# Kernel tuning notes

Hardware: AMD Instinct MI355X
Metric: run time of the kernel (lower is better)

The kernel has to match this reference:

```python
import jax, jax.numpy as jnp
import numpy as np

B, N, S, D1, D2 = 8, 8192, 2048, 128, 256
MLP = [256, 128]
IN_CH = D1 + D2
EPS_INTERP = 1e-8
EPS_BN = 1e-5


def setup_inputs() -> dict:
    key = jax.random.key(0)
    ks = jax.random.split(key, 12)
    inp = {
        "xyz1": jax.random.normal(ks[0], (B, 3, N), dtype=jnp.float32),
        "xyz2": jax.random.normal(ks[1], (B, 3, S), dtype=jnp.float32),
        "points1": jax.random.normal(ks[2], (B, D1, N), dtype=jnp.float32),
        "points2": jax.random.normal(ks[3], (B, D2, S), dtype=jnp.float32),
    }
    # Conv1d(k=1) weights are [out, in]; BN has gamma/beta per channel.
    last = IN_CH
    for i, oc in enumerate(MLP):
        inp[f"W{i}"] = jax.random.normal(ks[4 + 2 * i], (oc, last), dtype=jnp.float32) * (1.0 / np.sqrt(last))
        inp[f"b{i}"] = jnp.zeros((oc,), dtype=jnp.float32)
        inp[f"g{i}"] = jnp.ones((oc,), dtype=jnp.float32)
        inp[f"be{i}"] = jnp.zeros((oc,), dtype=jnp.float32)
        last = oc
    return inp


def _interpolate(xyz1, xyz2, points2):
    # xyz1: [B,3,N] -> [B,N,3]; xyz2: [B,3,S] -> [B,S,3]; points2: [B,D2,S] -> [B,S,D2]
    x1 = jnp.transpose(xyz1, (0, 2, 1))
    x2 = jnp.transpose(xyz2, (0, 2, 1))
    p2 = jnp.transpose(points2, (0, 2, 1))
    # squared distances [B,N,S]
    dists = (jnp.sum(x1 * x1, -1)[:, :, None]
             - 2.0 * jnp.einsum("bnc,bsc->bns", x1, x2)
             + jnp.sum(x2 * x2, -1)[:, None, :])
    neg_d, idx = jax.lax.top_k(-dists, 3)         # 3 nearest neighbors
    d = -neg_d                                     # [B,N,3]
    recip = 1.0 / (d + EPS_INTERP)
    weight = recip / jnp.sum(recip, axis=2, keepdims=True)
    gathered = jax.vmap(lambda p, i: p[i])(p2, idx)   # [B,N,3,D2]
    return jnp.sum(gathered * weight[..., None], axis=2)  # [B,N,D2]


def _conv_bn_relu(x, W, b, g, be):
    # x: [B,C,N]; 1x1 conv == channel GEMM
    y = jnp.einsum("oc,bcn->bon", W, x) + b[None, :, None]
    mean = jnp.mean(y, axis=(0, 2), keepdims=True)
    var = jnp.mean((y - mean) ** 2, axis=(0, 2), keepdims=True)  # biased, torch BN train
    y = (y - mean) * jax.lax.rsqrt(var + EPS_BN)
    y = y * g[None, :, None] + be[None, :, None]
    return jax.nn.relu(y)


def reference(xyz1, xyz2, points1, points2, W0, b0, g0, be0, W1, b1, g1, be1):
    interp = _interpolate(xyz1, xyz2, points2)               # [B,N,D2]
    p1 = jnp.transpose(points1, (0, 2, 1))                    # [B,N,D1]
    new_points = jnp.concatenate([p1, interp], axis=-1)       # [B,N,D1+D2]
    new_points = jnp.transpose(new_points, (0, 2, 1))         # [B,D1+D2,N]
    new_points = _conv_bn_relu(new_points, W0, b0, g0, be0)
    new_points = _conv_bn_relu(new_points, W1, b1, g1, be1)
    return new_points
```

## Files before the change

### kernel.cpp

```cpp
#include <hip/hip_runtime.h>

typedef unsigned short ushort_t;
typedef __bf16 bf16x8 __attribute__((ext_vector_type(8)));
typedef float floatx4 __attribute__((ext_vector_type(4)));
typedef unsigned short ushort8_t __attribute__((ext_vector_type(8)));

#define B_ 8
#define N_ 8192
#define S_ 2048
#define D1_ 128
#define D2_ 256
#define INCH_ 384
#define M_ 65536

#define ASYNC_CP16(g, l)                                                  \
  __builtin_amdgcn_global_load_lds(                                       \
      (const __attribute__((address_space(1))) void*)(g),                 \
      (__attribute__((address_space(3))) void*)(l), 16, 0, 0)

constexpr size_t OFF_STATS = 0;
constexpr size_t OFF_W0B   = 8192;
constexpr size_t OFF_W1B   = 204800;
constexpr size_t OFF_X2P   = 270336;
constexpr size_t OFF_P2T   = 532480;
constexpr size_t OFF_XC    = 8921088;
constexpr size_t OFF_Y1    = 59252736;
constexpr size_t OFF_PS0   = OFF_P2T;
constexpr size_t OFF_PQ0   = OFF_P2T + 1048576;
constexpr size_t OFF_PS1   = OFF_P2T + 2097152;
constexpr size_t OFF_PQ1   = OFF_P2T + 2621440;

__device__ __forceinline__ ushort_t f2bf(float f) {
  __bf16 h = (__bf16)f;
  union { __bf16 h; ushort_t u; } v;
  v.h = h;
  return v.u;
}
__device__ __forceinline__ float bf2f(ushort_t h) {
  return __uint_as_float(((unsigned int)h) << 16);
}

__device__ __forceinline__ void ins3(float e, int s,
                                     float& c0, float& c1, float& c2,
                                     int& i0, int& i1, int& i2) {
  bool l0 = e < c0, l1 = e < c1, l2 = e < c2;
  float nf0 = fminf(e, c0);
  float nf1 = __builtin_amdgcn_fmed3f(e, c0, c1);
  float nf2 = __builtin_amdgcn_fmed3f(e, c1, c2);
  i2 = l1 ? i1 : (l2 ? s : i2);
  i1 = l0 ? i0 : (l1 ? s : i1);
  i0 = l0 ? s : i0;
  c0 = nf0; c1 = nf1; c2 = nf2;
}

__global__ __launch_bounds__(256) void k_pre(const float* __restrict__ W0,
                                             const float* __restrict__ W1,
                                             const float* __restrict__ xyz2,
                                             const float* __restrict__ P2,
                                             const float* __restrict__ P1,
                                             ushort_t* __restrict__ W0b,
                                             ushort_t* __restrict__ W1b,
                                             float4* __restrict__ x2p,
                                             ushort_t* __restrict__ p2t,
                                             ushort_t* __restrict__ Xc) {
  __shared__ float t[32][33];
  const int blk = blockIdx.x;
  const int tid = threadIdx.x;
  if (blk < 576) {
    int i = blk * 256 + tid;
    if (i < 98304) {
      W0b[i] = f2bf(W0[i]);
    } else if (i < 131072) {
      W1b[i - 98304] = f2bf(W1[i - 98304]);
    } else {
      int idx = i - 131072;
      int b = idx >> 11, s = idx & (S_ - 1);
      const float* base = xyz2 + (size_t)b * 3 * S_;
      float x = base[s], y = base[S_ + s], z = base[2 * S_ + s];
      x2p[idx] = make_float4(x, y, z, 0.5f * (x * x + y * y + z * z));
    }
    return;
  }
  int tx = tid & 31, ty = tid >> 5;
  if (blk < 4672) {
    int idx = blk - 576;
    int s0 = (idx & 63) * 32;
    int c0 = ((idx >> 6) & 7) * 32;
    int b = idx >> 9;
#pragma unroll
    for (int j = 0; j < 4; j++) {
      int c = c0 + ty + j * 8;
      t[ty + j * 8][tx] = P2[((size_t)b * D2_ + c) * S_ + s0 + tx];
    }
    __syncthreads();
#pragma unroll
    for (int j = 0; j < 4; j++) {
      int s = s0 + ty + j * 8;
      p2t[((size_t)b * S_ + s) * D2_ + c0 + tx] = f2bf(t[tx][ty + j * 8]);
    }
  } else {
    int idx = blk - 4672;
    int n0 = (idx & 255) * 32;
    int c0 = ((idx >> 8) & 3) * 32;
    int b = idx >> 10;
#pragma unroll
    for (int j = 0; j < 4; j++) {
      int c = c0 + ty + j * 8;
      t[ty + j * 8][tx] = P1[((size_t)b * D1_ + c) * N_ + n0 + tx];
    }
    __syncthreads();
#pragma unroll
    for (int j = 0; j < 4; j++) {
      int n = n0 + ty + j * 8;
      Xc[((size_t)b * N_ + n) * INCH_ + c0 + tx] = f2bf(t[tx][ty + j * 8]);
    }
  }
}

__global__ __launch_bounds__(512, 8) void k_knn(const float* __restrict__ xyz1,
                                                const float4* __restrict__ x2p,
                                                const ushort_t* __restrict__ p2t,
                                                ushort_t* __restrict__ Xc) {
  __shared__ float4 xs[8 * 289];
  __shared__ float wsh[64 * 3];
  __shared__ int   ish[64 * 3];
  int t = threadIdx.x;
  int q0 = blockIdx.x * 64;
  int b = q0 >> 13;
  int n0 = q0 & (N_ - 1);
  for (int l = t; l < S_; l += 512)
    xs[(l >> 8) * 289 + (l & 255)] = x2p[(size_t)b * S_ + l];
  int sub = t & 7;
  int qg = t >> 3;
  int n = n0 + qg;
  float qx = xyz1[((size_t)b * 3 + 0) * N_ + n];
  float qy = xyz1[((size_t)b * 3 + 1) * N_ + n];
  float qz = xyz1[((size_t)b * 3 + 2) * N_ + n];
  float nrm1 = qx * qx + qy * qy + qz * qz;
  __syncthreads();
  const float4* bp = xs + sub * 289;
  float k0 = 3e38f, k1 = 3e38f, k2 = 3e38f, k3 = 3e38f;
#pragma unroll 4
  for (int i = 0; i < 256; ++i) {
    float4 P = bp[i];
    float e = fmaf(-qx, P.x, fmaf(-qy, P.y, fmaf(-qz, P.z, P.w)));
    float dd = fmaf(2.f, e, nrm1);
    unsigned int kb = (__float_as_uint(dd) & 0xFFFFFF00u) | (unsigned int)i;
    float k = __uint_as_float(kb);
    float n0_ = fminf(k, k0);
    float n1_ = __builtin_amdgcn_fmed3f(k, k0, k1);
    float n2_ = __builtin_amdgcn_fmed3f(k, k1, k2);
    float n3_ = __builtin_amdgcn_fmed3f(k, k2, k3);
    k0 = n0_; k1 = n1_; k2 = n2_; k3 = n3_;
  }
  float ed[4];
  int   si[4];
  {
    float kk[4] = {k0, k1, k2, k3};
#pragma unroll
    for (int c = 0; c < 4; ++c) {
      int loc = (int)(__float_as_uint(kk[c]) & 255u);
      float4 P = bp[loc];
      float e = fmaf(-qx, P.x, fmaf(-qy, P.y, fmaf(-qz, P.z, P.w)));
      ed[c] = fmaf(2.f, e, nrm1);
      si[c] = (sub << 8) + loc;
    }
  }
  float c0 = 3e38f, c1 = 3e38f, c2 = 3e38f;
  int i0 = 0, i1 = 0, i2 = 0;
#pragma unroll
  for (int c = 0; c < 4; ++c) ins3(ed[c], si[c], c0, c1, c2, i0, i1, i2);
#pragma unroll
  for (int d = 1; d < 8; d <<= 1) {
    float e0 = __shfl_xor(c0, d); int s0 = __shfl_xor(i0, d);
    float e1 = __shfl_xor(c1, d); int s1 = __shfl_xor(i1, d);
    float e2 = __shfl_xor(c2, d); int s2 = __shfl_xor(i2, d);
    ins3(e0, s0, c0, c1, c2, i0, i1, i2);
    ins3(e1, s1, c0, c1, c2, i0, i1, i2);
    ins3(e2, s2, c0, c1, c2, i0, i1, i2);
  }
  if (sub == 0) {
    float r0 = 1.f / (c0 + 1e-8f);
    float r1 = 1.f / (c1 + 1e-8f);
    float r2 = 1.f / (c2 + 1e-8f);
    float rs = 1.f / (r0 + r1 + r2);
    wsh[qg * 3 + 0] = r0 * rs; wsh[qg * 3 + 1] = r1 * rs; wsh[qg * 3 + 2] = r2 * rs;
    ish[qg * 3 + 0] = i0; ish[qg * 3 + 1] = i1; ish[qg * 3 + 2] = i2;
  }
  __syncthreads();
  int lane = t & 63, grp = t >> 6;
  size_t sbase2 = (size_t)b * S_;
#pragma unroll 2
  for (int it = 0; it < 8; ++it) {
    int ql = it * 8 + grp;
    int q = q0 + ql;
    float w0 = wsh[ql * 3 + 0], w1 = wsh[ql * 3 + 1], w2 = wsh[ql * 3 + 2];
    int j0 = ish[ql * 3 + 0], j1 = ish[ql * 3 + 1], j2 = ish[ql * 3 + 2];
    ushort4 a0 = *(const ushort4*)&p2t[(sbase2 + j0) * D2_ + lane * 4];
    ushort4 a1 = *(const ushort4*)&p2t[(sbase2 + j1) * D2_ + lane * 4];
    ushort4 a2 = *(const ushort4*)&p2t[(sbase2 + j2) * D2_ + lane * 4];
    ushort4 o;
    o.x = f2bf(w0 * bf2f(a0.x) + w1 * bf2f(a1.x) + w2 * bf2f(a2.x));
    o.y = f2bf(w0 * bf2f(a0.y) + w1 * bf2f(a1.y) + w2 * bf2f(a2.y));
    o.z = f2bf(w0 * bf2f(a0.z) + w1 * bf2f(a1.z) + w2 * bf2f(a2.z));
    o.w = f2bf(w0 * bf2f(a0.w) + w1 * bf2f(a1.w) + w2 * bf2f(a2.w));
    *(ushort4*)&Xc[(size_t)q * INCH_ + D1_ + lane * 4] = o;
  }
}

__global__ __launch_bounds__(256) void k_redstats(const float* __restrict__ ps,
                                                  const float* __restrict__ pq,
                                                  float* __restrict__ sum,
                                                  float* __restrict__ ssq,
                                                  int ncols, int nrows) {
  __shared__ float ls[4], lq[4];
  int col = blockIdx.x;
  int t = threadIdx.x;
  float s = 0.f, q = 0.f;
  for (int r = t; r < nrows; r += 256) {
    s += ps[(size_t)r * ncols + col];
    q += pq[(size_t)r * ncols + col];
  }
#pragma unroll
  for (int d = 1; d < 64; d <<= 1) {
    s += __shfl_xor(s, d);
    q += __shfl_xor(q, d);
  }
  if ((t & 63) == 0) { ls[t >> 6] = s; lq[t >> 6] = q; }
  __syncthreads();
  if (t == 0) {
    sum[col] = ls[0] + ls[1] + ls[2] + ls[3];
    ssq[col] = lq[0] + lq[1] + lq[2] + lq[3];
  }
}

__global__ __launch_bounds__(256, 4) void k_gemm1(const ushort_t* __restrict__ A,
                                                  const ushort_t* __restrict__ Bw,
                                                  ushort_t* __restrict__ Cc,
                                                  float* __restrict__ psum,
                                                  float* __restrict__ pssq) {
  __shared__ __align__(16) char g1buf[20480];
  __shared__ float red_s[2][256], red_q[2][256];
  ushort_t* As = (ushort_t*)g1buf;
  ushort_t* Bs = (ushort_t*)(g1buf + 4096);
  ushort_t* cs = (ushort_t*)g1buf;
  const int tid = threadIdx.x;
  const int m0 = blockIdx.x * 64;
  const int wave = tid >> 6;
  const int wuni = __builtin_amdgcn_readfirstlane(wave);
  const int lane = tid & 63;
  const int quad = lane >> 4;
  const int l16 = lane & 15;
  const int wrow = (wave >> 1) * 32;
  const int wcol = (wave & 1) * 128;
  const int arow = tid >> 2, aseg = tid & 3;
  floatx4 acc[2][8];
#pragma unroll
  for (int i = 0; i < 2; i++)
#pragma unroll
    for (int j = 0; j < 8; j++) acc[i][j] = (floatx4){0.f, 0.f, 0.f, 0.f};

  for (int k0 = 0; k0 < INCH_; k0 += 32) {
    ASYNC_CP16(&A[(size_t)(m0 + arow) * INCH_ + k0 + aseg * 8], &As[wuni * 512]);
#pragma unroll
    for (int it = 0; it < 4; it++) {
      int l = tid + it * 256;
      int row = l >> 2, seg = l & 3;
      ASYNC_CP16(&Bw[(size_t)row * INCH_ + k0 + seg * 8], &Bs[it * 2048 + wuni * 512]);
    }
    __syncthreads();
    bf16x8 af[2];
#pragma unroll
    for (int mt = 0; mt < 2; mt++) af[mt] = *(const bf16x8*)&As[(wrow + mt * 16 + l16) * 32 + quad * 8];
#pragma unroll
    for (int half = 0; half < 2; half++) {
      bf16x8 bfr[4];
#pragma unroll
      for (int j = 0; j < 4; j++) {
        int nt = half * 4 + j;
        bfr[j] = *(const bf16x8*)&Bs[(wcol + nt * 16 + l16) * 32 + quad * 8];
      }
#pragma unroll
      for (int mt = 0; mt < 2; mt++)
#pragma unroll
        for (int j = 0; j < 4; j++)
          acc[mt][half * 4 + j] =
              __builtin_amdgcn_mfma_f32_16x16x32_bf16(af[mt], bfr[j], acc[mt][half * 4 + j], 0, 0, 0);
    }
    __syncthreads();
  }
#pragma unroll
  for (int nt = 0; nt < 8; nt++) {
    float s = 0.f, s2 = 0.f;
#pragma unroll
    for (int mt = 0; mt < 2; mt++)
#pragma unroll
      for (int i = 0; i < 4; i++) {
        float v = acc[mt][nt][i];
        s += v;
        s2 = fmaf(v, v, s2);
      }
    s += __shfl_xor(s, 16);  s2 += __shfl_xor(s2, 16);
    s += __shfl_xor(s, 32);  s2 += __shfl_xor(s2, 32);
    if (quad == 0) {
      int col = wcol + nt * 16 + l16;
      red_s[wave >> 1][col] = s;
      red_q[wave >> 1][col] = s2;
    }
  }
#pragma unroll
  for (int h = 0; h < 2; ++h) {
    __syncthreads();
    if ((wave & 1) == h) {
#pragma unroll
      for (int mt = 0; mt < 2; mt++)
#pragma unroll
        for (int i = 0; i < 4; i++) {
          int rl = wrow + mt * 16 + quad * 4 + i;
#pragma unroll
          for (int nt = 0; nt < 8; nt++)
            cs[rl * 136 + nt * 16 + l16] = f2bf(acc[mt][nt][i]);
        }
    }
    __syncthreads();
#pragma unroll
    for (int v = 0; v < 4; ++v) {
      int idx = v * 256 + tid;
      int row = idx >> 4;
      int c8 = (idx & 15) * 8;
      ushort8_t val = *(const ushort8_t*)&cs[row * 136 + c8];
      *(ushort8_t*)&Cc[(size_t)(m0 + row) * 256 + h * 128 + c8] = val;
    }
  }
  __syncthreads();
  {
    psum[(size_t)blockIdx.x * 256 + tid] = red_s[0][tid] + red_s[1][tid];
    pssq[(size_t)blockIdx.x * 256 + tid] = red_q[0][tid] + red_q[1][tid];
  }
}

__global__ __launch_bounds__(256, 4) void k_gemm2t(const ushort_t* __restrict__ Y1,
                                                   const ushort_t* __restrict__ Bw,
                                                   const float* __restrict__ sum0,
                                                   const float* __restrict__ ssq0,
                                                   const float* __restrict__ g0,
                                                   const float* __restrict__ be0,
                                                   ushort_t* __restrict__ Y2t,
                                                   float* __restrict__ psum,
                                                   float* __restrict__ pssq) {
  __shared__ __align__(16) char ubuf[64 * 129 * 4];
  __shared__ float scs[256], shs[256];
  __shared__ float red_s[2][128], red_q[2][128];
  ushort_t* As = (ushort_t*)ubuf;
  ushort_t* Bs = (ushort_t*)(ubuf + 4096);
  float* tb = (float*)ubuf;
  const int tid = threadIdx.x;
  const int m0 = blockIdx.x * 64;
  const int b = m0 >> 13;
  const int n0 = m0 & (N_ - 1);
  const int wave = tid >> 6;
  const int wuni = __builtin_amdgcn_readfirstlane(wave);
  const int lane = tid & 63;
  const int quad = lane >> 4;
  const int l16 = lane & 15;
  const int wrow = (wave >> 1) * 32;
  const int wcol = (wave & 1) * 64;
  {
    float mean = sum0[tid] * (1.f / 65536.f);
    float var = ssq0[tid] * (1.f / 65536.f) - mean * mean;
    float sc = rsqrtf(var + 1e-5f) * g0[tid];
    scs[tid] = sc;
    shs[tid] = be0[tid] - mean * sc;
  }
  floatx4 acc[2][4];
#pragma unroll
  for (int i = 0; i < 2; i++)
#pragma unroll
    for (int j = 0; j < 4; j++) acc[i][j] = (floatx4){0.f, 0.f, 0.f, 0.f};
  __syncthreads();

  const int arow = tid >> 2, aseg = tid & 3;
  for (int k0 = 0; k0 < 256; k0 += 32) {
#pragma unroll
    for (int it = 0; it < 2; it++) {
      int l = tid + it * 256;
      int row = l >> 2, seg = l & 3;
      ASYNC_CP16(&Bw[(size_t)row * 256 + k0 + seg * 8], &Bs[it * 2048 + wuni * 512]);
    }
    {
      ushort4 y01 = *(const ushort4*)&Y1[(size_t)(m0 + arow) * 256 + k0 + aseg * 8];
      ushort4 y23 = *(const ushort4*)&Y1[(size_t)(m0 + arow) * 256 + k0 + aseg * 8 + 4];
      int c = k0 + aseg * 8;
      ushort4 o0, o1;
      o0.x = f2bf(fmaxf(fmaf(bf2f(y01.x), scs[c + 0], shs[c + 0]), 0.f));
      o0.y = f2bf(fmaxf(fmaf(bf2f(y01.y), scs[c + 1], shs[c + 1]), 0.f));
      o0.z = f2bf(fmaxf(fmaf(bf2f(y01.z), scs[c + 2], shs[c + 2]), 0.f));
      o0.w = f2bf(fmaxf(fmaf(bf2f(y01.w), scs[c + 3], shs[c + 3]), 0.f));
      o1.x = f2bf(fmaxf(fmaf(bf2f(y23.x), scs[c + 4], shs[c + 4]), 0.f));
      o1.y = f2bf(fmaxf(fmaf(bf2f(y23.y), scs[c + 5], shs[c + 5]), 0.f));
      o1.z = f2bf(fmaxf(fmaf(bf2f(y23.z), scs[c + 6], shs[c + 6]), 0.f));
      o1.w = f2bf(fmaxf(fmaf(bf2f(y23.w), scs[c + 7], shs[c + 7]), 0.f));
      *(ushort4*)&As[arow * 32 + aseg * 8] = o0;
      *(ushort4*)&As[arow * 32 + aseg * 8 + 4] = o1;
    }
    __syncthreads();
    bf16x8 af[2], bfr[4];
#pragma unroll
    for (int mt = 0; mt < 2; mt++) af[mt] = *(const bf16x8*)&As[(wrow + mt * 16 + l16) * 32 + quad * 8];
#pragma unroll
    for (int nt = 0; nt < 4; nt++) bfr[nt] = *(const bf16x8*)&Bs[(wcol + nt * 16 + l16) * 32 + quad * 8];
#pragma unroll
    for (int mt = 0; mt < 2; mt++)
#pragma unroll
      for (int nt = 0; nt < 4; nt++)
        acc[mt][nt] = __builtin_amdgcn_mfma_f32_16x16x32_bf16(af[mt], bfr[nt], acc[mt][nt], 0, 0, 0);
    __syncthreads();
  }
#pragma unroll
  for (int nt = 0; nt < 4; nt++) {
    float s = 0.f, s2 = 0.f;
#pragma unroll
    for (int mt = 0; mt < 2; mt++)
#pragma unroll
      for (int i = 0; i < 4; i++) {
        float v = acc[mt][nt][i];
        s += v;
        s2 = fmaf(v, v, s2);
      }
    s += __shfl_xor(s, 16);  s2 += __shfl_xor(s2, 16);
    s += __shfl_xor(s, 32);  s2 += __shfl_xor(s2, 32);
    if (quad == 0) {
      int col = wcol + nt * 16 + l16;
      red_s[wave >> 1][col] = s;
      red_q[wave >> 1][col] = s2;
    }
  }
#pragma unroll
  for (int mt = 0; mt < 2; mt++)
#pragma unroll
    for (int i = 0; i < 4; i++) {
      int rl = wrow + mt * 16 + quad * 4 + i;
#pragma unroll
      for (int nt = 0; nt < 4; nt++) {
        int col = wcol + nt * 16 + l16;
        tb[rl * 129 + col] = acc[mt][nt][i];
      }
    }
  __syncthreads();
  if (tid < 128) {
    psum[(size_t)blockIdx.x * 128 + tid] = red_s[0][tid] + red_s[1][tid];
    pssq[(size_t)blockIdx.x * 128 + tid] = red_q[0][tid] + red_q[1][tid];
  }
#pragma unroll
  for (int v = 0; v < 4; ++v) {
    int idx = v * 256 + tid;
    int c = idx >> 3;
    int j8 = (idx & 7) * 8;
    ushort8_t val;
#pragma unroll
    for (int k = 0; k < 8; ++k) val[k] = f2bf(tb[(j8 + k) * 129 + c]);
    *(ushort8_t*)&Y2t[((size_t)(b * 128 + c)) * N_ + n0 + j8] = val;
  }
}

__global__ __launch_bounds__(256) void k_out2(const ushort_t* __restrict__ Y2t,
                                              const float* __restrict__ sum1,
                                              const float* __restrict__ ssq1,
                                              const float* __restrict__ g1,
                                              const float* __restrict__ be1,
                                              float* __restrict__ out) {
  __shared__ float sc1[128], sh1[128];
  int tid = threadIdx.x;
  if (tid < 128) {
    float mean = sum1[tid] * (1.f / 65536.f);
    float var = ssq1[tid] * (1.f / 65536.f) - mean * mean;
    float sc = rsqrtf(var + 1e-5f) * g1[tid];
    sc1[tid] = sc;
    sh1[tid] = be1[tid] - mean * sc;
  }
  __syncthreads();
#pragma unroll
  for (int it = 0; it < 4; ++it) {
    int fid = (it * 2048 + blockIdx.x) * 256 + tid;
    int r = fid >> 11;
    int c = r & 127;
    int n4 = (fid & 2047) * 4;
    ushort4 y = *(const ushort4*)&Y2t[((size_t)r << 13) + n4];
    float sc = sc1[c], sh = sh1[c];
    float4 v;
    v.x = fmaxf(fmaf(bf2f(y.x), sc, sh), 0.f);
    v.y = fmaxf(fmaf(bf2f(y.y), sc, sh), 0.f);
    v.z = fmaxf(fmaf(bf2f(y.z), sc, sh), 0.f);
    v.w = fmaxf(fmaf(bf2f(y.w), sc, sh), 0.f);
    *(float4*)&out[((size_t)r << 13) + n4] = v;
  }
}

extern "C" void kernel_launch(void* const* d_in, const int* in_sizes, int n_in,
                              void* d_out, int out_size, void* d_ws, size_t ws_size,
                              hipStream_t stream) {
  const float* xyz1    = (const float*)d_in[0];
  const float* xyz2    = (const float*)d_in[1];
  const float* points1 = (const float*)d_in[2];
  const float* points2 = (const float*)d_in[3];
  const float* W0 = (const float*)d_in[4];
  const float* g0 = (const float*)d_in[6];
  const float* be0 = (const float*)d_in[7];
  const float* W1 = (const float*)d_in[8];
  const float* g1 = (const float*)d_in[10];
  const float* be1 = (const float*)d_in[11];
  float* out = (float*)d_out;
  char* ws = (char*)d_ws;

  float* sum0   = (float*)(ws + OFF_STATS);
  float* ssq0   = sum0 + 256;
  float* sum1   = sum0 + 512;
  float* ssq1   = sum0 + 640;
  ushort_t* W0b = (ushort_t*)(ws + OFF_W0B);
  ushort_t* W1b = (ushort_t*)(ws + OFF_W1B);
  float4* x2p   = (float4*)(ws + OFF_X2P);
  ushort_t* p2t = (ushort_t*)(ws + OFF_P2T);
  ushort_t* Xc  = (ushort_t*)(ws + OFF_XC);
  ushort_t* Y1b = (ushort_t*)(ws + OFF_Y1);
  ushort_t* Y2t = (ushort_t*)(ws + OFF_XC);
  float* psum0  = (float*)(ws + OFF_PS0);
  float* pssq0  = (float*)(ws + OFF_PQ0);
  float* psum1  = (float*)(ws + OFF_PS1);
  float* pssq1  = (float*)(ws + OFF_PQ1);

  k_pre<<<12864, 256, 0, stream>>>(W0, W1, xyz2, points2, points1,
                                   W0b, W1b, x2p, p2t, Xc);
  k_knn<<<1024, 512, 0, stream>>>(xyz1, x2p, p2t, Xc);
  k_gemm1<<<1024, 256, 0, stream>>>(Xc, W0b, Y1b, psum0, pssq0);
  k_redstats<<<256, 256, 0, stream>>>(psum0, pssq0, sum0, ssq0, 256, 1024);
  k_gemm2t<<<1024, 256, 0, stream>>>(Y1b, W1b, sum0, ssq0, g0, be0,
                                     Y2t, psum1, pssq1);
  k_redstats<<<128, 256, 0, stream>>>(psum1, pssq1, sum1, ssq1, 128, 1024);
  k_out2<<<2048, 256, 0, stream>>>(Y2t, sum1, ssq1, g1, be1, out);
}
```

Baseline: 221.2 us.

## Fuse points1 transpose/convert into GEMM1 A-load and widen vector accesses

The points1 transpose and bf16 conversion is removed from the preprocessing kernel. GEMM1 now reads the first 128 input channels straight from fp32 points1 and converts them into shared memory, which avoids writing and re-reading that slice of the concat buffer. This adds strided scalar global loads inside the GEMM k-loop. Separately, k_knn's occupancy hint drops from 8 to 4 and its unroll rises to 8, and gemm2's A-staging and k_out2 now use 8-wide vector loads.

```diff
diff --git a/kernel.cpp b/kernel.cpp
--- a/kernel.cpp
+++ b/kernel.cpp
@@ -57,12 +57,10 @@
                                              const float* __restrict__ W1,
                                              const float* __restrict__ xyz2,
                                              const float* __restrict__ P2,
-                                             const float* __restrict__ P1,
                                              ushort_t* __restrict__ W0b,
                                              ushort_t* __restrict__ W1b,
                                              float4* __restrict__ x2p,
-                                             ushort_t* __restrict__ p2t,
-                                             ushort_t* __restrict__ Xc) {
+                                             ushort_t* __restrict__ p2t) {
   __shared__ float t[32][33];
   const int blk = blockIdx.x;
   const int tid = threadIdx.x;
@@ -82,42 +80,24 @@
     return;
   }
   int tx = tid & 31, ty = tid >> 5;
-  if (blk < 4672) {
-    int idx = blk - 576;
-    int s0 = (idx & 63) * 32;
-    int c0 = ((idx >> 6) & 7) * 32;
-    int b = idx >> 9;
-#pragma unroll
-    for (int j = 0; j < 4; j++) {
-      int c = c0 + ty + j * 8;
-      t[ty + j * 8][tx] = P2[((size_t)b * D2_ + c) * S_ + s0 + tx];
-    }
-    __syncthreads();
-#pragma unroll
-    for (int j = 0; j < 4; j++) {
-      int s = s0 + ty + j * 8;
-      p2t[((size_t)b * S_ + s) * D2_ + c0 + tx] = f2bf(t[tx][ty + j * 8]);
-    }
-  } else {
-    int idx = blk - 4672;
-    int n0 = (idx & 255) * 32;
-    int c0 = ((idx >> 8) & 3) * 32;
-    int b = idx >> 10;
-#pragma unroll
-    for (int j = 0; j < 4; j++) {
-      int c = c0 + ty + j * 8;
-      t[ty + j * 8][tx] = P1[((size_t)b * D1_ + c) * N_ + n0 + tx];
-    }
-    __syncthreads();
-#pragma unroll
-    for (int j = 0; j < 4; j++) {
-      int n = n0 + ty + j * 8;
-      Xc[((size_t)b * N_ + n) * INCH_ + c0 + tx] = f2bf(t[tx][ty + j * 8]);
-    }
-  }
-}
-
-__global__ __launch_bounds__(512, 8) void k_knn(const float* __restrict__ xyz1,
+  int idx = blk - 576;
+  int s0 = (idx & 63) * 32;
+  int c0 = ((idx >> 6) & 7) * 32;
+  int b = idx >> 9;
+#pragma unroll
+  for (int j = 0; j < 4; j++) {
+    int c = c0 + ty + j * 8;
+    t[ty + j * 8][tx] = P2[((size_t)b * D2_ + c) * S_ + s0 + tx];
+  }
+  __syncthreads();
+#pragma unroll
+  for (int j = 0; j < 4; j++) {
+    int s = s0 + ty + j * 8;
+    p2t[((size_t)b * S_ + s) * D2_ + c0 + tx] = f2bf(t[tx][ty + j * 8]);
+  }
+}
+
+__global__ __launch_bounds__(512, 4) void k_knn(const float* __restrict__ xyz1,
                                                 const float4* __restrict__ x2p,
                                                 const ushort_t* __restrict__ p2t,
                                                 ushort_t* __restrict__ Xc) {
@@ -140,7 +120,7 @@
   __syncthreads();
   const float4* bp = xs + sub * 289;
   float k0 = 3e38f, k1 = 3e38f, k2 = 3e38f, k3 = 3e38f;
-#pragma unroll 4
+#pragma unroll 8
   for (int i = 0; i < 256; ++i) {
     float4 P = bp[i];
     float e = fmaf(-qx, P.x, fmaf(-qy, P.y, fmaf(-qz, P.z, P.w)));
@@ -236,6 +216,7 @@
 
 __global__ __launch_bounds__(256, 4) void k_gemm1(const ushort_t* __restrict__ A,
                                                   const ushort_t* __restrict__ Bw,
+                                                  const float* __restrict__ P1g,
                                                   ushort_t* __restrict__ Cc,
                                                   float* __restrict__ psum,
                                                   float* __restrict__ pssq) {
@@ -246,6 +227,8 @@
   ushort_t* cs = (ushort_t*)g1buf;
   const int tid = threadIdx.x;
   const int m0 = blockIdx.x * 64;
+  const int bb = m0 >> 13;
+  const int n0g = m0 & (N_ - 1);
   const int wave = tid >> 6;
   const int wuni = __builtin_amdgcn_readfirstlane(wave);
   const int lane = tid & 63;
@@ -261,7 +244,15 @@
     for (int j = 0; j < 8; j++) acc[i][j] = (floatx4){0.f, 0.f, 0.f, 0.f};
 
   for (int k0 = 0; k0 < INCH_; k0 += 32) {
-    ASYNC_CP16(&A[(size_t)(m0 + arow) * INCH_ + k0 + aseg * 8], &As[wuni * 512]);
+    if (k0 < D1_) {
+      ushort8_t w;
+#pragma unroll
+      for (int j = 0; j < 8; j++)
+        w[j] = f2bf(P1g[((size_t)bb * D1_ + k0 + aseg * 8 + j) * N_ + n0g + arow]);
+      *(ushort8_t*)&As[arow * 32 + aseg * 8] = w;
+    } else {
+      ASYNC_CP16(&A[(size_t)(m0 + arow) * INCH_ + k0 + aseg * 8], &As[wuni * 512]);
+    }
 #pragma unroll
     for (int it = 0; it < 4; it++) {
       int l = tid + it * 256;
@@ -388,20 +379,13 @@
       ASYNC_CP16(&Bw[(size_t)row * 256 + k0 + seg * 8], &Bs[it * 2048 + wuni * 512]);
     }
     {
-      ushort4 y01 = *(const ushort4*)&Y1[(size_t)(m0 + arow) * 256 + k0 + aseg * 8];
-      ushort4 y23 = *(const ushort4*)&Y1[(size_t)(m0 + arow) * 256 + k0 + aseg * 8 + 4];
+      ushort8_t y = *(const ushort8_t*)&Y1[(size_t)(m0 + arow) * 256 + k0 + aseg * 8];
       int c = k0 + aseg * 8;
-      ushort4 o0, o1;
-      o0.x = f2bf(fmaxf(fmaf(bf2f(y01.x), scs[c + 0], shs[c + 0]), 0.f));
-      o0.y = f2bf(fmaxf(fmaf(bf2f(y01.y), scs[c + 1], shs[c + 1]), 0.f));
-      o0.z = f2bf(fmaxf(fmaf(bf2f(y01.z), scs[c + 2], shs[c + 2]), 0.f));
-      o0.w = f2bf(fmaxf(fmaf(bf2f(y01.w), scs[c + 3], shs[c + 3]), 0.f));
-      o1.x = f2bf(fmaxf(fmaf(bf2f(y23.x), scs[c + 4], shs[c + 4]), 0.f));
-      o1.y = f2bf(fmaxf(fmaf(bf2f(y23.y), scs[c + 5], shs[c + 5]), 0.f));
-      o1.z = f2bf(fmaxf(fmaf(bf2f(y23.z), scs[c + 6], shs[c + 6]), 0.f));
-      o1.w = f2bf(fmaxf(fmaf(bf2f(y23.w), scs[c + 7], shs[c + 7]), 0.f));
-      *(ushort4*)&As[arow * 32 + aseg * 8] = o0;
-      *(ushort4*)&As[arow * 32 + aseg * 8 + 4] = o1;
+      ushort8_t o;
+#pragma unroll
+      for (int j = 0; j < 8; j++)
+        o[j] = f2bf(fmaxf(fmaf(bf2f(y[j]), scs[c + j], shs[c + j]), 0.f));
+      *(ushort8_t*)&As[arow * 32 + aseg * 8] = o;
     }
     __syncthreads();
     bf16x8 af[2], bfr[4];
@@ -480,19 +464,24 @@
   }
   __syncthreads();
 #pragma unroll
-  for (int it = 0; it < 4; ++it) {
+  for (int it = 0; it < 2; ++it) {
     int fid = (it * 2048 + blockIdx.x) * 256 + tid;
-    int r = fid >> 11;
+    int r = fid >> 10;
     int c = r & 127;
-    int n4 = (fid & 2047) * 4;
-    ushort4 y = *(const ushort4*)&Y2t[((size_t)r << 13) + n4];
+    int n8 = (fid & 1023) * 8;
+    ushort8_t y = *(const ushort8_t*)&Y2t[((size_t)r << 13) + n8];
     float sc = sc1[c], sh = sh1[c];
-    float4 v;
-    v.x = fmaxf(fmaf(bf2f(y.x), sc, sh), 0.f);
-    v.y = fmaxf(fmaf(bf2f(y.y), sc, sh), 0.f);
-    v.z = fmaxf(fmaf(bf2f(y.z), sc, sh), 0.f);
-    v.w = fmaxf(fmaf(bf2f(y.w), sc, sh), 0.f);
-    *(float4*)&out[((size_t)r << 13) + n4] = v;
+    float4 v0, v1;
+    v0.x = fmaxf(fmaf(bf2f(y[0]), sc, sh), 0.f);
+    v0.y = fmaxf(fmaf(bf2f(y[1]), sc, sh), 0.f);
+    v0.z = fmaxf(fmaf(bf2f(y[2]), sc, sh), 0.f);
+    v0.w = fmaxf(fmaf(bf2f(y[3]), sc, sh), 0.f);
+    v1.x = fmaxf(fmaf(bf2f(y[4]), sc, sh), 0.f);
+    v1.y = fmaxf(fmaf(bf2f(y[5]), sc, sh), 0.f);
+    v1.z = fmaxf(fmaf(bf2f(y[6]), sc, sh), 0.f);
+    v1.w = fmaxf(fmaf(bf2f(y[7]), sc, sh), 0.f);
+    *(float4*)&out[((size_t)r << 13) + n8] = v0;
+    *(float4*)&out[((size_t)r << 13) + n8 + 4] = v1;
   }
 }
 
@@ -528,10 +517,10 @@
   float* psum1  = (float*)(ws + OFF_PS1);
   float* pssq1  = (float*)(ws + OFF_PQ1);
 
-  k_pre<<<12864, 256, 0, stream>>>(W0, W1, xyz2, points2, points1,
-                                   W0b, W1b, x2p, p2t, Xc);
+  k_pre<<<4672, 256, 0, stream>>>(W0, W1, xyz2, points2,
+                                  W0b, W1b, x2p, p2t);
   k_knn<<<1024, 512, 0, stream>>>(xyz1, x2p, p2t, Xc);
-  k_gemm1<<<1024, 256, 0, stream>>>(Xc, W0b, Y1b, psum0, pssq0);
+  k_gemm1<<<1024, 256, 0, stream>>>(Xc, W0b, points1, Y1b, psum0, pssq0);
   k_redstats<<<256, 256, 0, stream>>>(psum0, pssq0, sum0, ssq0, 256, 1024);
   k_gemm2t<<<1024, 256, 0, stream>>>(Y1b, W1b, sum0, ssq0, g0, be0,
                                      Y2t, psum1, pssq1);
```

New measurement: 219.4 us. Within noise of the previous version (-0.8%).
